# Performance work log

Measured on AMD Instinct MI355X. Metric: run time of the kernel, lower is better.

The kernel has to match this reference:

```python
import jax, jax.numpy as jnp
import numpy as np

SIZE = 4096
NB = 16            # nr_blocks_per_row
NDROP = 8          # nr_blocks_to_drop_per_row
BATCH = 8192
BLOCK = SIZE // NB # 256


def _block_mask():
    # latin_square(n): S[i,j] = ((i+j) mod n) + 1, values 1..n, each once per row/col
    i = np.arange(NB)
    S = ((i[:, None] + i[None, :]) % NB) + 1
    m = S > NDROP  # keep NB-NDROP blocks per row
    mask = np.repeat(np.repeat(m, BLOCK, axis=0), BLOCK, axis=1)
    return jnp.asarray(mask)  # [SIZE, SIZE] bool


def setup_inputs() -> dict:
    key = jax.random.key(0)
    kx, kw, kb = jax.random.split(key, 3)
    x = jax.random.normal(kx, (BATCH, SIZE), dtype=jnp.float32)
    # kaiming_normal_ default: fan_in mode, relu gain -> std = sqrt(2/fan_in)
    weight = jax.random.normal(kw, (SIZE, SIZE), dtype=jnp.float32) * jnp.sqrt(2.0 / SIZE)
    # uniform(-1,1) scaled by sqrt(1/size)
    bias = jax.random.uniform(kb, (SIZE,), minval=-1.0, maxval=1.0, dtype=jnp.float32) * jnp.sqrt(1.0 / SIZE)
    mask = _block_mask()
    return {"x": x, "weight": weight, "bias": bias, "mask": mask}


def reference(x, weight, bias, mask):
    # x @ (mask * weight).T + bias
    w = jnp.where(mask, weight, jnp.zeros((), dtype=weight.dtype))
    return x @ w.T + bias
```

## Files before the change

### kernel.cpp

```cpp
#include <hip/hip_runtime.h>
#include <hip/hip_bf16.h>
#include <stdint.h>


typedef __bf16 bf16x8 __attribute__((ext_vector_type(8)));
typedef float  f32x4  __attribute__((ext_vector_type(4)));

#define AS1 __attribute__((address_space(1)))
#define AS3 __attribute__((address_space(3)))

__device__ __forceinline__ void async_cp16(const void* g, void* l) {
  __builtin_amdgcn_global_load_lds((const AS1 void*)g, (AS3 void*)l, 16, 0, 0);
}

__device__ __forceinline__ uint32_t pack_bf16(float a, float b) {
  uint32_t ua = __float_as_uint(a);
  ua += 0x7fffu + ((ua >> 16) & 1u);
  uint32_t ub = __float_as_uint(b);
  ub += 0x7fffu + ((ub >> 16) & 1u);
  return (ua >> 16) | (ub & 0xffff0000u);
}

__global__ __launch_bounds__(256) void cvt_f32_bf16(const float* __restrict__ in,
                                                    uint32_t* __restrict__ out,
                                                    int n8) {
  int i = blockIdx.x * 256 + threadIdx.x;
  if (i >= n8) return;
  const float4* p = (const float4*)in + (size_t)i * 2;
  float4 a = p[0];
  float4 b = p[1];
  uint4 r;
  r.x = pack_bf16(a.x, a.y);
  r.y = pack_bf16(a.z, a.w);
  r.z = pack_bf16(b.x, b.y);
  r.w = pack_bf16(b.z, b.w);
  ((uint4*)out)[i] = r;
}

__global__ __launch_bounds__(256, 2) void gemm_bs(
    const uint16_t* __restrict__ X,
    const uint16_t* __restrict__ W,
    const float* __restrict__ bias,
    float* __restrict__ out) {
  constexpr int K = 4096;
  __shared__ uint16_t sA[128 * 32];
  __shared__ uint16_t sB[128 * 32];

  const int tid = threadIdx.x;
  const int bn = blockIdx.x;
  const int bm = blockIdx.y;
  const int m0 = bm << 7;
  const int n0 = bn << 7;
  const int bi = bn >> 1;

  const int tr = tid >> 2;
  const int tc = (tid & 3) << 3;
  const uint16_t* gA0 = X + (size_t)(m0 + tr) * K + tc;
  const uint16_t* gA1 = X + (size_t)(m0 + 64 + tr) * K + tc;
  const uint16_t* gB0 = W + (size_t)(n0 + tr) * K + tc;
  const uint16_t* gB1 = W + (size_t)(n0 + 64 + tr) * K + tc;
  uint16_t* lA0 = sA + tid * 8;
  uint16_t* lA1 = sA + 2048 + tid * 8;
  uint16_t* lB0 = sB + tid * 8;
  uint16_t* lB1 = sB + 2048 + tid * 8;

  const int lane = tid & 63;
  const int wv = tid >> 6;
  const int wm = (wv >> 1) << 6;
  const int wn = (wv & 1) << 6;
  const int fr = lane & 15;
  const int fk = (lane >> 4) << 3;

  f32x4 acc[4][4];
#pragma unroll
  for (int i = 0; i < 4; ++i)
#pragma unroll
    for (int j = 0; j < 4; ++j)
      acc[i][j] = (f32x4){0.f, 0.f, 0.f, 0.f};

  for (int t = 0; t < 8; ++t) {
    const int kb = ((24 + t - bi) & 15) << 8;
#pragma unroll
    for (int u = 0; u < 8; ++u) {
      const int kg = kb + (u << 5);
      __syncthreads();
      async_cp16(gA0 + kg, lA0);
      async_cp16(gA1 + kg, lA1);
      async_cp16(gB0 + kg, lB0);
      async_cp16(gB1 + kg, lB1);
      __syncthreads();

      bf16x8 av[4], bv[4];
#pragma unroll
      for (int i = 0; i < 4; ++i)
        av[i] = *(const bf16x8*)(sA + ((wm + (i << 4) + fr) << 5) + fk);
#pragma unroll
      for (int j = 0; j < 4; ++j)
        bv[j] = *(const bf16x8*)(sB + ((wn + (j << 4) + fr) << 5) + fk);
#pragma unroll
      for (int i = 0; i < 4; ++i)
#pragma unroll
        for (int j = 0; j < 4; ++j)
          acc[i][j] = __builtin_amdgcn_mfma_f32_16x16x32_bf16(av[i], bv[j],
                                                              acc[i][j], 0, 0, 0);
    }
  }

  const int rq = (lane >> 4) << 2;
#pragma unroll
  for (int j = 0; j < 4; ++j) {
    const int c = n0 + wn + (j << 4) + fr;
    const float bz = bias[c];
#pragma unroll
    for (int i = 0; i < 4; ++i) {
      const int r0 = m0 + wm + (i << 4) + rq;
#pragma unroll
      for (int r = 0; r < 4; ++r)
        out[(size_t)(r0 + r) * 4096 + c] = acc[i][j][r] + bz;
    }
  }
}

extern "C" void kernel_launch(void* const* d_in, const int* in_sizes, int n_in,
                              void* d_out, int out_size, void* d_ws, size_t ws_size,
                              hipStream_t stream) {
  const float* x = (const float*)d_in[0];
  const float* w = (const float*)d_in[1];
  const float* bias = (const float*)d_in[2];
  float* out = (float*)d_out;

  uint16_t* xb = (uint16_t*)d_ws;
  uint16_t* wb = xb + (size_t)8192 * 4096;

  const int nx8 = (8192 * 4096) / 8;
  const int nw8 = (4096 * 4096) / 8;
  hipLaunchKernelGGL(cvt_f32_bf16, dim3(nx8 / 256), dim3(256), 0, stream,
                     x, (uint32_t*)xb, nx8);
  hipLaunchKernelGGL(cvt_f32_bf16, dim3(nw8 / 256), dim3(256), 0, stream,
                     w, (uint32_t*)wb, nw8);

  dim3 grid(32, 64);
  hipLaunchKernelGGL(gemm_bs, grid, dim3(256), 0, stream, xb, wb, bias, out);
}
```

Before: 488.8 us.

## Swizzle LDS layout, group-order tiles, fuse conversions, raise occupancy

XOR-swizzles the 16-byte chunk position within each 32-element LDS row so the fragment reads spread across banks instead of conflicting. The grid becomes a 1D launch with grouped ordering (8 M-tiles per group) to improve L2 reuse of weight tiles. The two f32-to-bf16 conversion kernels merge into one grid-stride launch, and the launch bound moves from 2 to 4 blocks per SM, which may push up register pressure or cause spills.

```diff
diff --git a/kernel.cpp b/kernel.cpp
--- a/kernel.cpp
+++ b/kernel.cpp
@@ -21,23 +21,31 @@
   return (ua >> 16) | (ub & 0xffff0000u);
 }
 
-__global__ __launch_bounds__(256) void cvt_f32_bf16(const float* __restrict__ in,
-                                                    uint32_t* __restrict__ out,
-                                                    int n8) {
-  int i = blockIdx.x * 256 + threadIdx.x;
-  if (i >= n8) return;
-  const float4* p = (const float4*)in + (size_t)i * 2;
-  float4 a = p[0];
-  float4 b = p[1];
-  uint4 r;
-  r.x = pack_bf16(a.x, a.y);
-  r.y = pack_bf16(a.z, a.w);
-  r.z = pack_bf16(b.x, b.y);
-  r.w = pack_bf16(b.z, b.w);
-  ((uint4*)out)[i] = r;
+__global__ __launch_bounds__(256) void cvt_both(const float* __restrict__ x,
+                                                const float* __restrict__ w,
+                                                uint32_t* __restrict__ xb,
+                                                uint32_t* __restrict__ wb,
+                                                int nx8, int ntot8) {
+  int stride = gridDim.x * 256;
+  for (int i = blockIdx.x * 256 + threadIdx.x; i < ntot8; i += stride) {
+    const float* src;
+    uint32_t* dst;
+    int j;
+    if (i < nx8) { src = x; dst = xb; j = i; }
+    else         { src = w; dst = wb; j = i - nx8; }
+    const float4* p = (const float4*)src + (size_t)j * 2;
+    float4 a = p[0];
+    float4 b = p[1];
+    uint4 r;
+    r.x = pack_bf16(a.x, a.y);
+    r.y = pack_bf16(a.z, a.w);
+    r.z = pack_bf16(b.x, b.y);
+    r.w = pack_bf16(b.z, b.w);
+    ((uint4*)dst)[j] = r;
+  }
 }
 
-__global__ __launch_bounds__(256, 2) void gemm_bs(
+__global__ __launch_bounds__(256, 4) void gemm_bs(
     const uint16_t* __restrict__ X,
     const uint16_t* __restrict__ W,
     const float* __restrict__ bias,
@@ -47,14 +55,20 @@
   __shared__ uint16_t sB[128 * 32];
 
   const int tid = threadIdx.x;
-  const int bn = blockIdx.x;
-  const int bm = blockIdx.y;
+
+  const int pid = blockIdx.x;
+  constexpr int NPN = 32;
+  constexpr int GRP = 8;
+  const int gid = pid / (GRP * NPN);
+  const int rem = pid % (GRP * NPN);
+  const int bm = gid * GRP + (rem % GRP);
+  const int bn = rem / GRP;
   const int m0 = bm << 7;
   const int n0 = bn << 7;
   const int bi = bn >> 1;
 
   const int tr = tid >> 2;
-  const int tc = (tid & 3) << 3;
+  const int tc = (((tid & 3) ^ (tr & 3)) << 3);
   const uint16_t* gA0 = X + (size_t)(m0 + tr) * K + tc;
   const uint16_t* gA1 = X + (size_t)(m0 + 64 + tr) * K + tc;
   const uint16_t* gB0 = W + (size_t)(n0 + tr) * K + tc;
@@ -69,7 +83,7 @@
   const int wm = (wv >> 1) << 6;
   const int wn = (wv & 1) << 6;
   const int fr = lane & 15;
-  const int fk = (lane >> 4) << 3;
+  const int fkp = (((lane >> 4) ^ (fr & 3)) << 3);
 
   f32x4 acc[4][4];
 #pragma unroll
@@ -93,10 +107,10 @@
       bf16x8 av[4], bv[4];
 #pragma unroll
       for (int i = 0; i < 4; ++i)
-        av[i] = *(const bf16x8*)(sA + ((wm + (i << 4) + fr) << 5) + fk);
+        av[i] = *(const bf16x8*)(sA + ((wm + (i << 4) + fr) << 5) + fkp);
 #pragma unroll
       for (int j = 0; j < 4; ++j)
-        bv[j] = *(const bf16x8*)(sB + ((wn + (j << 4) + fr) << 5) + fk);
+        bv[j] = *(const bf16x8*)(sB + ((wn + (j << 4) + fr) << 5) + fkp);
 #pragma unroll
       for (int i = 0; i < 4; ++i)
 #pragma unroll
@@ -134,11 +148,10 @@
 
   const int nx8 = (8192 * 4096) / 8;
   const int nw8 = (4096 * 4096) / 8;
-  hipLaunchKernelGGL(cvt_f32_bf16, dim3(nx8 / 256), dim3(256), 0, stream,
-                     x, (uint32_t*)xb, nx8);
-  hipLaunchKernelGGL(cvt_f32_bf16, dim3(nw8 / 256), dim3(256), 0, stream,
-                     w, (uint32_t*)wb, nw8);
+  const int ntot8 = nx8 + nw8;
+  hipLaunchKernelGGL(cvt_both, dim3(2048), dim3(256), 0, stream,
+                     x, w, (uint32_t*)xb, (uint32_t*)wb, nx8, ntot8);
 
-  dim3 grid(32, 64);
-  hipLaunchKernelGGL(gemm_bs, grid, dim3(256), 0, stream, xb, wb, bias, out);
+  hipLaunchKernelGGL(gemm_bs, dim3(2048), dim3(256), 0, stream,
+                     (const uint16_t*)xb, (const uint16_t*)wb, bias, out);
 }
```

Result: slower. 546.1 us (+11.7%).
